# Kernel tuning notes

Measured on AMD Instinct MI355X. Metric: run time of the kernel, lower is better.

## Reference

```python
import jax, jax.numpy as jnp
import numpy as np

N, E, G = 20000, 320000, 1000
F_NODE, F_EDGE, HID, HEADS, NCLS = 12, 4, 64, 4, 4


def setup_inputs() -> dict:
    key = jax.random.key(0)
    ks = iter(jax.random.split(key, 64))

    def rn(shape, s=0.1):
        return jax.random.normal(next(ks), shape, jnp.float32) * s

    inp = {
        "x": rn((N, F_NODE), 1.0),
        "edge_index": jax.random.randint(next(ks), (2, E), 0, N, dtype=jnp.int32),
        "edge_attr": rn((E, F_EDGE), 1.0),
        "batch": jnp.sort(jax.random.randint(next(ks), (N,), 0, G, dtype=jnp.int32)),
    }
    # GATv2 layer params: lin_l (W,b), lin_r (W,b), lin_edge (W, no bias), att, out bias
    for i, (cin, H) in enumerate([(F_NODE, HEADS), (HID * HEADS, HEADS), (HID * HEADS, 1)], 1):
        d = H * HID
        inp[f"Wl{i}"] = rn((cin, d))
        inp[f"bl{i}"] = rn((d,))
        inp[f"Wr{i}"] = rn((cin, d))
        inp[f"br{i}"] = rn((d,))
        inp[f"We{i}"] = rn((F_EDGE, d))
        inp[f"att{i}"] = rn((H, HID))
        inp[f"bias{i}"] = rn((d,))
    inp["mW1"] = rn((HID, 32)); inp["mb1"] = rn((32,))
    inp["mW2"] = rn((32, 16)); inp["mb2"] = rn((16,))
    inp["mW3"] = rn((16, NCLS)); inp["mb3"] = rn((NCLS,))
    return inp


def gatv2(x, src, dst, ea, Wl, bl, Wr, br, We, att, bias, H):
    # PyG GATv2Conv (share_weights=False, negative_slope=0.2, concat=True, eval mode)
    xl = (x @ Wl + bl).reshape(N, H, HID)   # source transform
    xr = (x @ Wr + br).reshape(N, H, HID)   # target transform
    ee = (ea @ We).reshape(E, H, HID)       # edge embedding
    z = jax.nn.leaky_relu(xl[src] + xr[dst] + ee, 0.2)  # [E,H,C]
    logits = jnp.einsum("ehc,hc->eh", z, att)
    m = jax.ops.segment_max(logits, dst, num_segments=N)  # per-dest max
    ex = jnp.exp(logits - m[dst])
    denom = jax.ops.segment_sum(ex, dst, num_segments=N)
    alpha = ex / (denom[dst] + 1e-16)                      # segment softmax
    msg = (xl[src] * alpha[:, :, None]).reshape(E, H * HID)
    out = jax.ops.segment_sum(msg, dst, num_segments=N)
    return out + bias


def reference(x, edge_index, edge_attr, batch,
              Wl1, bl1, Wr1, br1, We1, att1, bias1,
              Wl2, bl2, Wr2, br2, We2, att2, bias2,
              Wl3, bl3, Wr3, br3, We3, att3, bias3,
              mW1, mb1, mW2, mb2, mW3, mb3):
    src, dst = edge_index[0], edge_index[1]
    h = jax.nn.elu(gatv2(x, src, dst, edge_attr, Wl1, bl1, Wr1, br1, We1, att1, bias1, HEADS))
    h = jax.nn.elu(gatv2(h, src, dst, edge_attr, Wl2, bl2, Wr2, br2, We2, att2, bias2, HEADS))
    h = gatv2(h, src, dst, edge_attr, Wl3, bl3, Wr3, br3, We3, att3, bias3, 1)  # [N,HID]
    # global mean pool
    sums = jax.ops.segment_sum(h, batch, num_segments=G)
    cnt = jax.ops.segment_sum(jnp.ones((N, 1), h.dtype), batch, num_segments=G)
    g = sums / jnp.maximum(cnt, 1.0)
    # MLP head (dropout disabled, eval mode)
    g = jax.nn.relu(g @ mW1 + mb1)
    g = jax.nn.relu(g @ mW2 + mb2)
    return g @ mW3 + mb3
```

## Files before the change

kernel.cpp:

```cpp
#include <hip/hip_runtime.h>
#include <hip/hip_bf16.h>

#define NNODES 20000
#define NEDGES 320000
#define NGRAPH 1000

typedef __hip_bfloat16 bf16;
typedef unsigned short u16;
typedef short short8 __attribute__((ext_vector_type(8)));
typedef float f32x4 __attribute__((ext_vector_type(4)));

__device__ __forceinline__ float b2f(bf16 x) { return __bfloat162float(x); }
__device__ __forceinline__ float bu2f(u16 u) { return __uint_as_float(((unsigned)u) << 16); }
__device__ __forceinline__ u16 f2bu(float v) {
    __hip_bfloat16 b = __float2bfloat16(v);
    return *reinterpret_cast<u16*>(&b);
}

__device__ __forceinline__ int idx_at(const void* p, int i, int is64) {
    return is64 ? (int)((const long long*)p)[i] : ((const int*)p)[i];
}

__device__ __forceinline__ float raw_at(const void* p, size_t i, bool isbf) {
    return isbf ? b2f(((const bf16*)p)[i]) : ((const float*)p)[i];
}

static inline char* align16(char* p) {
    return (char*)(((uintptr_t)p + 15) & ~(uintptr_t)15);
}

__global__ void sniff_all(const void* __restrict__ x, const void* __restrict__ ei,
                          const void* __restrict__ batch, int* __restrict__ flags) {
    __shared__ int sb[4];
    if (threadIdx.x < 4) sb[threadIdx.x] = 0;
    __syncthreads();
    int gb = 0, gf = 0, ze = 0, zb = 0;
    for (int i = threadIdx.x; i < 8192; i += blockDim.x) {
        float vb = b2f(((const bf16*)x)[i]);
        float vf = ((const float*)x)[i];
        if (fabsf(vb) < 1e4f) gb++;
        if (fabsf(vf) < 1e4f) gf++;
        if (((const int*)ei)[2 * i + 1] == 0) ze++;
        if (((const int*)batch)[2 * i + 1] == 0) zb++;
    }
    atomicAdd(&sb[0], gb); atomicAdd(&sb[1], gf);
    atomicAdd(&sb[2], ze); atomicAdd(&sb[3], zb);
    __syncthreads();
    if (threadIdx.x == 0) {
        flags[0] = (sb[0] >= sb[1]) ? 1 : 0;
        flags[1] = (sb[2] > 6000) ? 1 : 0;
        flags[2] = (sb[3] > 6000) ? 1 : 0;
    }
}

struct Segs {
    const void* src[29];
    int off[30];
};

__device__ __forceinline__ void wtp_store(u16* __restrict__ dst, const void* __restrict__ src,
                                          int K, int N, int i, bool isbf) {
    int j = i & 7;
    int lane = (i >> 3) & 63;
    int rest = i >> 9;
    int KB = K >> 5;
    int tile = rest / KB, kbi = rest - tile * KB;
    int l16 = lane & 15, quad = lane >> 4;
    int n = tile * 16 + l16;
    int kk = kbi * 32 + quad * 8 + j;
    dst[i] = f2bu(raw_at(src, (size_t)kk * N + n, isbf));
}

__global__ void preprocess(Segs S, const int* __restrict__ flags,
                           float* __restrict__ conv, int total,
                           u16* __restrict__ eah,
                           u16* __restrict__ wt2l, u16* __restrict__ wt2r,
                           u16* __restrict__ wt3l, u16* __restrict__ wt3r,
                           int* __restrict__ deg, float* __restrict__ poolcnt) {
    int i = blockIdx.x * blockDim.x + threadIdx.x;
    bool isbf = flags[0] != 0;
    if (i < total) {
        int lo = 0, hi = 29;
        while (hi - lo > 1) {
            int mid = (lo + hi) >> 1;
            if (i >= S.off[mid]) lo = mid; else hi = mid;
        }
        conv[i] = raw_at(S.src[lo], i - S.off[lo], isbf);
        return;
    }
    i -= total;
    if (i < NEDGES * 4) {
        eah[i] = isbf ? ((const u16*)S.src[1])[i] : f2bu(((const float*)S.src[1])[i]);
        return;
    }
    i -= NEDGES * 4;
    if (i < 65536) { wtp_store(wt2l, S.src[9],  256, 256, i, isbf); return; }
    i -= 65536;
    if (i < 65536) { wtp_store(wt2r, S.src[11], 256, 256, i, isbf); return; }
    i -= 65536;
    if (i < 16384) { wtp_store(wt3l, S.src[16], 256, 64, i, isbf); return; }
    i -= 16384;
    if (i < 16384) { wtp_store(wt3r, S.src[18], 256, 64, i, isbf); return; }
    i -= 16384;
    if (i < NNODES) { deg[i] = 0; return; }
    i -= NNODES;
    if (i < NGRAPH * 65) poolcnt[i] = 0.f;
}

__global__ void csr_hist(const void* __restrict__ ei, const int* __restrict__ flags,
                         int* __restrict__ deg) {
    int e = blockIdx.x * blockDim.x + threadIdx.x;
    if (e >= NEDGES) return;
    atomicAdd(&deg[idx_at(ei, NEDGES + e, flags[1])], 1);
}

__global__ void csr_scan(const int* __restrict__ deg, int* __restrict__ rowptr,
                         int* __restrict__ cursor) {
    __shared__ int wsum[16];
    __shared__ int wpre[16];
    const int t = threadIdx.x;
    const int wid = t >> 6, lane = t & 63;
    const int base = t * 20;
    int loc[20];
    int s = 0;
#pragma unroll
    for (int j = 0; j < 20; j++) {
        int i = base + j;
        int v = (i < NNODES) ? deg[i] : 0;
        loc[j] = s;
        s += v;
    }
    int incl = s;
#pragma unroll
    for (int o = 1; o < 64; o <<= 1) {
        int n = __shfl_up(incl, o);
        if (lane >= o) incl += n;
    }
    if (lane == 63) wsum[wid] = incl;
    __syncthreads();
    if (wid == 0 && lane < 16) {
        int v = wsum[lane];
        int inc2 = v;
#pragma unroll
        for (int o = 1; o < 16; o <<= 1) {
            int n = __shfl_up(inc2, o);
            if (lane >= o) inc2 += n;
        }
        wpre[lane] = inc2 - v;
    }
    __syncthreads();
    int excl = wpre[wid] + incl - s;
#pragma unroll
    for (int j = 0; j < 20; j++) {
        int i = base + j;
        if (i < NNODES) { rowptr[i] = excl + loc[j]; cursor[i] = excl + loc[j]; }
    }
    if (t == 1023) rowptr[NNODES] = excl + s;
}

__global__ void csr_scatter(const void* __restrict__ ei, const int* __restrict__ flags,
                            int* __restrict__ cursor, int2* __restrict__ csr) {
    int e = blockIdx.x * blockDim.x + threadIdx.x;
    if (e >= NEDGES) return;
    const int i64 = flags[1];
    int src = idx_at(ei, e, i64), dst = idx_at(ei, NEDGES + e, i64);
    int pos = atomicAdd(&cursor[dst], 1);
    csr[pos] = make_int2(src, e);
}

template <int TM, int CIN, int DOUT, bool GUARD>
__global__ __launch_bounds__(256, 2) void lin_gemm(
        const float* __restrict__ X,
        const float* __restrict__ Wl, const float* __restrict__ bl,
        const float* __restrict__ Wr, const float* __restrict__ br,
        u16* __restrict__ XL, float* __restrict__ XR) {
    constexpr int CPT = DOUT / 4;
    constexpr int RG = 256 / CPT;
    constexpr int M = RG * TM;
    __shared__ float xs[M * CIN];

    const int t = threadIdx.x;
    const int ct = t % CPT;
    const int rg = t / CPT;
    const int c0 = ct * 4;
    const int r0 = blockIdx.x * M;

    constexpr int C4 = CIN / 4;
    for (int i = t; i < M * C4; i += 256) {
        int r = i / C4, j = i - r * C4;
        float4 v = make_float4(0.f, 0.f, 0.f, 0.f);
        if (!GUARD || (r0 + r) < NNODES)
            v = *(const float4*)&X[(size_t)(r0 + r) * CIN + j * 4];
        *(float4*)&xs[r * CIN + j * 4] = v;
    }
    __syncthreads();

    float4 accL[TM], accR[TM];
#pragma unroll
    for (int m = 0; m < TM; m++) {
        accL[m] = make_float4(0.f, 0.f, 0.f, 0.f);
        accR[m] = make_float4(0.f, 0.f, 0.f, 0.f);
    }
    const float* xbase = &xs[rg * TM * CIN];
#pragma unroll 4
    for (int k = 0; k < CIN; k++) {
        const float4 wl = *(const float4*)&Wl[k * DOUT + c0];
        const float4 wr = *(const float4*)&Wr[k * DOUT + c0];
#pragma unroll
        for (int m = 0; m < TM; m++) {
            float xv = xbase[m * CIN + k];
            accL[m].x = fmaf(xv, wl.x, accL[m].x);
            accL[m].y = fmaf(xv, wl.y, accL[m].y);
            accL[m].z = fmaf(xv, wl.z, accL[m].z);
            accL[m].w = fmaf(xv, wl.w, accL[m].w);
            accR[m].x = fmaf(xv, wr.x, accR[m].x);
            accR[m].y = fmaf(xv, wr.y, accR[m].y);
            accR[m].z = fmaf(xv, wr.z, accR[m].z);
            accR[m].w = fmaf(xv, wr.w, accR[m].w);
        }
    }

    const float4 b4l = *(const float4*)&bl[c0];
    const float4 b4r = *(const float4*)&br[c0];
#pragma unroll
    for (int m = 0; m < TM; m++) {
        int row = r0 + rg * TM + m;
        if (GUARD && row >= NNODES) continue;
        float l0 = accL[m].x + b4l.x, l1 = accL[m].y + b4l.y;
        float l2 = accL[m].z + b4l.z, l3 = accL[m].w + b4l.w;
        uint2 pk;
        pk.x = (unsigned)f2bu(l0) | ((unsigned)f2bu(l1) << 16);
        pk.y = (unsigned)f2bu(l2) | ((unsigned)f2bu(l3) << 16);
        *(uint2*)&XL[(size_t)row * DOUT + c0] = pk;
        float4 r4;
        r4.x = accR[m].x + b4r.x; r4.y = accR[m].y + b4r.y;
        r4.z = accR[m].z + b4r.z; r4.w = accR[m].w + b4r.w;
        *(float4*)&XR[(size_t)row * DOUT + c0] = r4;
    }
}

template <int N>
__global__ __launch_bounds__(256) void lin_gemm_mfma(
        const float* __restrict__ X,
        const u16* __restrict__ WlP, const float* __restrict__ bl,
        const u16* __restrict__ WrP, const float* __restrict__ br,
        u16* __restrict__ XL, float* __restrict__ XR) {
    constexpr int K = 256;
    constexpr int KB = K / 32;
    constexpr int NTW = N / 64;
    constexpr int XSTR = 264;
    __shared__ u16 xhi[16 * XSTR];
    __shared__ u16 xlo[16 * XSTR];

    const int t = threadIdx.x;
    const int w = t >> 6, lane = t & 63;
    const int quad = lane >> 4, l16 = lane & 15;
    const int m0 = blockIdx.x * 16;
    const int nbase = w * (N / 4);

    for (int idx = t; idx < 16 * 64; idx += 256) {
        int r = idx >> 6, c4 = idx & 63;
        float4 v = *(const float4*)&X[(size_t)(m0 + r) * K + c4 * 4];
        float f[4] = {v.x, v.y, v.z, v.w};
        ushort4 hi, lo;
        u16 h;
        h = f2bu(f[0]); hi.x = h; lo.x = f2bu(f[0] - bu2f(h));
        h = f2bu(f[1]); hi.y = h; lo.y = f2bu(f[1] - bu2f(h));
        h = f2bu(f[2]); hi.z = h; lo.z = f2bu(f[2] - bu2f(h));
        h = f2bu(f[3]); hi.w = h; lo.w = f2bu(f[3] - bu2f(h));
        *(ushort4*)&xhi[r * XSTR + c4 * 4] = hi;
        *(ushort4*)&xlo[r * XSTR + c4 * 4] = lo;
    }
    __syncthreads();

    f32x4 accL[NTW], accR[NTW];
#pragma unroll
    for (int i = 0; i < NTW; i++) {
        accL[i] = (f32x4){0.f, 0.f, 0.f, 0.f};
        accR[i] = (f32x4){0.f, 0.f, 0.f, 0.f};
    }

    const int abase = l16 * XSTR + quad * 8;
#pragma unroll
    for (int kbi = 0; kbi < KB; kbi++) {
        short8 ahi = *(const short8*)&xhi[abase + kbi * 32];
        short8 alo = *(const short8*)&xlo[abase + kbi * 32];
#pragma unroll
        for (int i = 0; i < NTW; i++) {
            int tg = (nbase >> 4) + i;
            size_t off = ((size_t)(tg * KB + kbi) * 64 + lane) * 8;
            short8 bL = *(const short8*)&WlP[off];
            short8 bR = *(const short8*)&WrP[off];
            accL[i] = __builtin_amdgcn_mfma_f32_16x16x32_bf16(ahi, bL, accL[i], 0, 0, 0);
            accL[i] = __builtin_amdgcn_mfma_f32_16x16x32_bf16(alo, bL, accL[i], 0, 0, 0);
            accR[i] = __builtin_amdgcn_mfma_f32_16x16x32_bf16(ahi, bR, accR[i], 0, 0, 0);
            accR[i] = __builtin_amdgcn_mfma_f32_16x16x32_bf16(alo, bR, accR[i], 0, 0, 0);
        }
    }

#pragma unroll
    for (int i = 0; i < NTW; i++) {
        int col = nbase + i * 16 + l16;
        float bLv = bl[col], bRv = br[col];
#pragma unroll
        for (int r = 0; r < 4; r++) {
            int row = m0 + quad * 4 + r;
            XL[(size_t)row * N + col] = f2bu(accL[i][r] + bLv);
            XR[(size_t)row * N + col] = accR[i][r] + bRv;
        }
    }
}

template <int H, bool ELU, bool POOLF>
__global__ __launch_bounds__(H * 64, 4) void gat_agg(
                        const int* __restrict__ rowptr, const int2* __restrict__ csr,
                        const u16* __restrict__ XL, const float* __restrict__ XR,
                        const u16* __restrict__ eah,
                        const float* __restrict__ We, const float* __restrict__ att,
                        const float* __restrict__ bias, float* __restrict__ out,
                        const void* __restrict__ batch, const int* __restrict__ flags,
                        float* __restrict__ pool, float* __restrict__ cnt) {
    const int Dout = H * 64;
    const int dst = blockIdx.x;
    const int t = threadIdx.x;
    const int h = t >> 6;
    const int lane = t & 63;
    const int g = lane >> 4;
    const int k = lane & 15;
    const int c0 = h * 64 + k * 4;

    const float4 w0 = *(const float4*)&We[0 * Dout + c0];
    const float4 w1 = *(const float4*)&We[1 * Dout + c0];
    const float4 w2 = *(const float4*)&We[2 * Dout + c0];
    const float4 w3 = *(const float4*)&We[3 * Dout + c0];
    const float4 at = *(const float4*)&att[c0];
    const float4 xr = *(const float4*)&XR[dst * Dout + c0];

    const int i0 = rowptr[dst], i1 = rowptr[dst + 1];
    const int niter = (i1 - i0 + 3) >> 2;

    float l = 0.f;
    float4 acc = make_float4(0.f, 0.f, 0.f, 0.f);

#define GAT_EDGE_BODY(E_IDX)                                                     \
    {                                                                            \
        int e_ = (E_IDX);                                                        \
        bool valid_ = e_ < i1;                                                   \
        int2 se_ = csr[valid_ ? e_ : i0];                                        \
        uint2 xu_ = *(const uint2*)&XL[se_.x * Dout + c0];                       \
        uint2 au_ = *(const uint2*)&eah[se_.y * 4];                              \
        float xl0_ = __uint_as_float(xu_.x << 16);                               \
        float xl1_ = __uint_as_float(xu_.x & 0xffff0000u);                       \
        float xl2_ = __uint_as_float(xu_.y << 16);                               \
        float xl3_ = __uint_as_float(xu_.y & 0xffff0000u);                       \
        float A0_ = __uint_as_float(au_.x << 16);                                \
        float A1_ = __uint_as_float(au_.x & 0xffff0000u);                        \
        float A2_ = __uint_as_float(au_.y << 16);                                \
        float A3_ = __uint_as_float(au_.y & 0xffff0000u);                        \
        float z0_ = fmaf(A0_, w0.x, fmaf(A1_, w1.x, fmaf(A2_, w2.x, fmaf(A3_, w3.x, xl0_ + xr.x)))); \
        float z1_ = fmaf(A0_, w0.y, fmaf(A1_, w1.y, fmaf(A2_, w2.y, fmaf(A3_, w3.y, xl1_ + xr.y)))); \
        float z2_ = fmaf(A0_, w0.z, fmaf(A1_, w1.z, fmaf(A2_, w2.z, fmaf(A3_, w3.z, xl2_ + xr.z)))); \
        float z3_ = fmaf(A0_, w0.w, fmaf(A1_, w1.w, fmaf(A2_, w2.w, fmaf(A3_, w3.w, xl3_ + xr.w)))); \
        z0_ = fmaxf(z0_, 0.2f * z0_);                                            \
        z1_ = fmaxf(z1_, 0.2f * z1_);                                            \
        z2_ = fmaxf(z2_, 0.2f * z2_);                                            \
        z3_ = fmaxf(z3_, 0.2f * z3_);                                            \
        float v_ = fmaf(z3_, at.w, fmaf(z2_, at.z, fmaf(z1_, at.y, z0_ * at.x))); \
        v_ += __shfl_xor(v_, 1);                                                 \
        v_ += __shfl_xor(v_, 2);                                                 \
        v_ += __shfl_xor(v_, 4);                                                 \
        v_ += __shfl_xor(v_, 8);                                                 \
        float p_ = valid_ ? __expf(v_) : 0.f;                                    \
        l += p_;                                                                 \
        acc.x = fmaf(p_, xl0_, acc.x);                                           \
        acc.y = fmaf(p_, xl1_, acc.y);                                           \
        acc.z = fmaf(p_, xl2_, acc.z);                                           \
        acc.w = fmaf(p_, xl3_, acc.w);                                           \
    }

    int it = 0;
    for (; it + 2 <= niter; it += 2) {
        int eb = i0 + g + it * 4;
        GAT_EDGE_BODY(eb)
        GAT_EDGE_BODY(eb + 4)
    }
    if (it < niter) {
        GAT_EDGE_BODY(i0 + g + it * 4)
    }
#undef GAT_EDGE_BODY

    l += __shfl_xor(l, 16);      l += __shfl_xor(l, 32);
    acc.x += __shfl_xor(acc.x, 16); acc.x += __shfl_xor(acc.x, 32);
    acc.y += __shfl_xor(acc.y, 16); acc.y += __shfl_xor(acc.y, 32);
    acc.z += __shfl_xor(acc.z, 16); acc.z += __shfl_xor(acc.z, 32);
    acc.w += __shfl_xor(acc.w, 16); acc.w += __shfl_xor(acc.w, 32);

    if (g == 0) {
        float inv = 1.f / (l + 1e-16f);
        const float4 b4 = *(const float4*)&bias[c0];
        float o0 = fmaf(acc.x, inv, b4.x);
        float o1 = fmaf(acc.y, inv, b4.y);
        float o2 = fmaf(acc.z, inv, b4.z);
        float o3 = fmaf(acc.w, inv, b4.w);
        if (ELU) {
            o0 = o0 > 0.f ? o0 : expf(o0) - 1.f;
            o1 = o1 > 0.f ? o1 : expf(o1) - 1.f;
            o2 = o2 > 0.f ? o2 : expf(o2) - 1.f;
            o3 = o3 > 0.f ? o3 : expf(o3) - 1.f;
        }
        if (POOLF) {
            int b = idx_at(batch, dst, flags[2]);
            atomicAdd(&pool[b * 64 + c0 + 0], o0);
            atomicAdd(&pool[b * 64 + c0 + 1], o1);
            atomicAdd(&pool[b * 64 + c0 + 2], o2);
            atomicAdd(&pool[b * 64 + c0 + 3], o3);
            if (lane == 0) atomicAdd(&cnt[b], 1.f);
        } else {
            *(float4*)&out[dst * Dout + c0] = make_float4(o0, o1, o2, o3);
        }
    }
}

__global__ void mlp_head(const float* __restrict__ pool, const float* __restrict__ cnt,
                         const float* __restrict__ mW1, const float* __restrict__ mb1,
                         const float* __restrict__ mW2, const float* __restrict__ mb2,
                         const float* __restrict__ mW3, const float* __restrict__ mb3,
                         float* __restrict__ out) {
    __shared__ float g[64], s1[32], s2[16];
    int b = blockIdx.x, t = threadIdx.x;
    float c = fmaxf(cnt[b], 1.f);
    g[t] = pool[b * 64 + t] / c;
    __syncthreads();
    if (t < 32) {
        float a = 0.f;
        for (int k = 0; k < 64; k++) a = fmaf(g[k], mW1[k * 32 + t], a);
        s1[t] = fmaxf(a + mb1[t], 0.f);
    }
    __syncthreads();
    if (t < 16) {
        float a = 0.f;
        for (int k = 0; k < 32; k++) a = fmaf(s1[k], mW2[k * 16 + t], a);
        s2[t] = fmaxf(a + mb2[t], 0.f);
    }
    __syncthreads();
    if (t < 4) {
        float a = 0.f;
        for (int k = 0; k < 16; k++) a = fmaf(s2[k], mW3[k * 4 + t], a);
        out[b * 4 + t] = a + mb3[t];
    }
}


extern "C" void kernel_launch(void* const* d_in, const int* in_sizes, int n_in,
                              void* d_out, int out_size, void* d_ws, size_t ws_size,
                              hipStream_t stream) {
    const void* ei    = d_in[1];
    const void* batch = d_in[3];

    int fidx[29];
    fidx[0] = 0;
    fidx[1] = 2;
    for (int i = 0; i < 21; i++) fidx[2 + i] = 4 + i;
    for (int i = 0; i < 6; i++) fidx[23 + i] = 25 + i;

    Segs S;
    int off = 0;
    for (int i = 0; i < 29; i++) {
        S.src[i] = d_in[fidx[i]];
        S.off[i] = off;
        off += in_sizes[fidx[i]];
    }
    S.off[29] = off;
    const int total = off;

    char* p = (char*)d_ws;
    int*   FLAGS  = (int*)p;                 p += 16;
    float* CONV   = (float*)p;               p += sizeof(float) * total;  p = align16(p);
    int*   DEG    = (int*)p;                 p += sizeof(int) * NNODES;
    int*   ROWPTR = (int*)p;                 p += sizeof(int) * (NNODES + 1);
    int*   CURSOR = (int*)p;                 p += sizeof(int) * (NNODES + 1);  p = align16(p);
    int2*  CSR    = (int2*)p;                p += sizeof(int2) * NEDGES;  p = align16(p);
    u16*   EAH    = (u16*)p;                 p += sizeof(u16) * NEDGES * 4;  p = align16(p);
    u16*   WT2L   = (u16*)p;                 p += sizeof(u16) * 256 * 256;
    u16*   WT2R   = (u16*)p;                 p += sizeof(u16) * 256 * 256;
    u16*   WT3L   = (u16*)p;                 p += sizeof(u16) * 64 * 256;
    u16*   WT3R   = (u16*)p;                 p += sizeof(u16) * 64 * 256;  p = align16(p);
    u16*   XLb    = (u16*)p;                 p += sizeof(u16) * NNODES * 256;  p = align16(p);
    float* XRb    = (float*)p;               p += sizeof(float) * NNODES * 256;
    float* ACC    = (float*)p;               p += sizeof(float) * NNODES * 256;
    float* POOL   = (float*)p;               p += sizeof(float) * NGRAPH * 64;
    float* CNT    = (float*)p;               p += sizeof(float) * NGRAPH;

    const float* CX  = CONV + S.off[0];
    const float* CP[21];
    for (int i = 0; i < 21; i++) CP[i] = CONV + S.off[2 + i];
    const float* CmW1 = CONV + S.off[23];
    const float* Cmb1 = CONV + S.off[24];
    const float* CmW2 = CONV + S.off[25];
    const float* Cmb2 = CONV + S.off[26];
    const float* CmW3 = CONV + S.off[27];
    const float* Cmb3 = CONV + S.off[28];

    sniff_all<<<1, 256, 0, stream>>>(d_in[0], ei, batch, FLAGS);
    int pre_total = total + NEDGES * 4 + 65536 * 2 + 16384 * 2 + NNODES + NGRAPH * 65;
    preprocess<<<(pre_total + 255) / 256, 256, 0, stream>>>(
        S, FLAGS, CONV, total, EAH, WT2L, WT2R, WT3L, WT3R, DEG, POOL);

    csr_hist<<<(NEDGES + 255) / 256, 256, 0, stream>>>(ei, FLAGS, DEG);
    csr_scan<<<1, 1024, 0, stream>>>(DEG, ROWPTR, CURSOR);
    csr_scatter<<<(NEDGES + 255) / 256, 256, 0, stream>>>(ei, FLAGS, CURSOR, CSR);

    lin_gemm<4, 12, 256, false><<<NNODES / 16, 256, 0, stream>>>(CX, CP[0], CP[1], CP[2], CP[3], XLb, XRb);
    gat_agg<4, true, false><<<NNODES, 256, 0, stream>>>(ROWPTR, CSR, XLb, XRb, EAH,
        CP[4], CP[5], CP[6], ACC, batch, FLAGS, POOL, CNT);

    lin_gemm_mfma<256><<<NNODES / 16, 256, 0, stream>>>(ACC, WT2L, CP[8], WT2R, CP[10], XLb, XRb);
    gat_agg<4, true, false><<<NNODES, 256, 0, stream>>>(ROWPTR, CSR, XLb, XRb, EAH,
        CP[11], CP[12], CP[13], ACC, batch, FLAGS, POOL, CNT);

    lin_gemm_mfma<64><<<NNODES / 16, 256, 0, stream>>>(ACC, WT3L, CP[15], WT3R, CP[17], XLb, XRb);
    gat_agg<1, false, true><<<NNODES, 64, 0, stream>>>(ROWPTR, CSR, XLb, XRb, EAH,
        CP[18], CP[19], CP[20], ACC, batch, FLAGS, POOL, CNT);

    mlp_head<<<NGRAPH, 64, 0, stream>>>(POOL, CNT, CmW1, Cmb1, CmW2, Cmb2, CmW3, Cmb3, (float*)d_out);
}
```

Baseline: 410.5 us.

## Use wavefront-per-node single-pass GATv2 aggregation for the 4-head layers

```diff
diff --git a/kernel.cpp b/kernel.cpp
--- a/kernel.cpp
+++ b/kernel.cpp
@@ -309,6 +309,86 @@
             XR[(size_t)row * N + col] = accR[i][r] + bRv;
         }
     }
+}
+
+template <bool ELU>
+__global__ __launch_bounds__(256, 4) void gat_agg_mw(
+        const int* __restrict__ rowptr, const int2* __restrict__ csr,
+        const u16* __restrict__ XL, const float* __restrict__ XR,
+        const u16* __restrict__ eah,
+        const float* __restrict__ We, const float* __restrict__ att,
+        const float* __restrict__ bias, float* __restrict__ out) {
+    const int w = threadIdx.x >> 6;
+    const int lane = threadIdx.x & 63;
+    const int dst = blockIdx.x * 4 + w;
+    const int c0 = lane * 4;
+
+    const float4 w0 = *(const float4*)&We[0 * 256 + c0];
+    const float4 w1 = *(const float4*)&We[1 * 256 + c0];
+    const float4 w2 = *(const float4*)&We[2 * 256 + c0];
+    const float4 w3 = *(const float4*)&We[3 * 256 + c0];
+    const float4 at = *(const float4*)&att[c0];
+    const float4 xr = *(const float4*)&XR[(size_t)dst * 256 + c0];
+
+    const int i0 = rowptr[dst], i1 = rowptr[dst + 1];
+
+    float l = 0.f;
+    float4 acc = make_float4(0.f, 0.f, 0.f, 0.f);
+
+    int2 sc = (i0 < i1) ? csr[i0] : make_int2(0, 0);
+    int2 sn = (i0 + 1 < i1) ? csr[i0 + 1] : sc;
+    uint2 xu = *(const uint2*)&XL[(size_t)sc.x * 256 + c0];
+    uint2 au = *(const uint2*)&eah[(size_t)sc.y * 4];
+
+    for (int e = i0; e < i1; ++e) {
+        int2 s2 = (e + 2 < i1) ? csr[e + 2] : sn;
+        uint2 xu_n = *(const uint2*)&XL[(size_t)sn.x * 256 + c0];
+        uint2 au_n = *(const uint2*)&eah[(size_t)sn.y * 4];
+
+        float xl0 = __uint_as_float(xu.x << 16);
+        float xl1 = __uint_as_float(xu.x & 0xffff0000u);
+        float xl2 = __uint_as_float(xu.y << 16);
+        float xl3 = __uint_as_float(xu.y & 0xffff0000u);
+        float A0 = __uint_as_float(au.x << 16);
+        float A1 = __uint_as_float(au.x & 0xffff0000u);
+        float A2 = __uint_as_float(au.y << 16);
+        float A3 = __uint_as_float(au.y & 0xffff0000u);
+        float z0 = fmaf(A0, w0.x, fmaf(A1, w1.x, fmaf(A2, w2.x, fmaf(A3, w3.x, xl0 + xr.x))));
+        float z1 = fmaf(A0, w0.y, fmaf(A1, w1.y, fmaf(A2, w2.y, fmaf(A3, w3.y, xl1 + xr.y))));
+        float z2 = fmaf(A0, w0.z, fmaf(A1, w1.z, fmaf(A2, w2.z, fmaf(A3, w3.z, xl2 + xr.z))));
+        float z3 = fmaf(A0, w0.w, fmaf(A1, w1.w, fmaf(A2, w2.w, fmaf(A3, w3.w, xl3 + xr.w))));
+        z0 = fmaxf(z0, 0.2f * z0);
+        z1 = fmaxf(z1, 0.2f * z1);
+        z2 = fmaxf(z2, 0.2f * z2);
+        z3 = fmaxf(z3, 0.2f * z3);
+        float v = fmaf(z3, at.w, fmaf(z2, at.z, fmaf(z1, at.y, z0 * at.x)));
+        v += __shfl_xor(v, 1);
+        v += __shfl_xor(v, 2);
+        v += __shfl_xor(v, 4);
+        v += __shfl_xor(v, 8);
+        float p = __expf(v);
+        l += p;
+        acc.x = fmaf(p, xl0, acc.x);
+        acc.y = fmaf(p, xl1, acc.y);
+        acc.z = fmaf(p, xl2, acc.z);
+        acc.w = fmaf(p, xl3, acc.w);
+
+        sn = s2; xu = xu_n; au = au_n;
+    }
+
+    float inv = 1.f / (l + 1e-16f);
+    const float4 b4 = *(const float4*)&bias[c0];
+    float o0 = fmaf(acc.x, inv, b4.x);
+    float o1 = fmaf(acc.y, inv, b4.y);
+    float o2 = fmaf(acc.z, inv, b4.z);
+    float o3 = fmaf(acc.w, inv, b4.w);
+    if (ELU) {
+        o0 = o0 > 0.f ? o0 : expf(o0) - 1.f;
+        o1 = o1 > 0.f ? o1 : expf(o1) - 1.f;
+        o2 = o2 > 0.f ? o2 : expf(o2) - 1.f;
+        o3 = o3 > 0.f ? o3 : expf(o3) - 1.f;
+    }
+    *(float4*)&out[(size_t)dst * 256 + c0] = make_float4(o0, o1, o2, o3);
 }
 
 template <int H, bool ELU, bool POOLF>
@@ -511,12 +591,12 @@
     csr_scatter<<<(NEDGES + 255) / 256, 256, 0, stream>>>(ei, FLAGS, CURSOR, CSR);
 
     lin_gemm<4, 12, 256, false><<<NNODES / 16, 256, 0, stream>>>(CX, CP[0], CP[1], CP[2], CP[3], XLb, XRb);
-    gat_agg<4, true, false><<<NNODES, 256, 0, stream>>>(ROWPTR, CSR, XLb, XRb, EAH,
-        CP[4], CP[5], CP[6], ACC, batch, FLAGS, POOL, CNT);
+    gat_agg_mw<true><<<NNODES / 4, 256, 0, stream>>>(ROWPTR, CSR, XLb, XRb, EAH,
+        CP[4], CP[5], CP[6], ACC);
 
     lin_gemm_mfma<256><<<NNODES / 16, 256, 0, stream>>>(ACC, WT2L, CP[8], WT2R, CP[10], XLb, XRb);
-    gat_agg<4, true, false><<<NNODES, 256, 0, stream>>>(ROWPTR, CSR, XLb, XRb, EAH,
-        CP[11], CP[12], CP[13], ACC, batch, FLAGS, POOL, CNT);
+    gat_agg_mw<true><<<NNODES / 4, 256, 0, stream>>>(ROWPTR, CSR, XLb, XRb, EAH,
+        CP[11], CP[12], CP[13], ACC);
 
     lin_gemm_mfma<64><<<NNODES / 16, 256, 0, stream>>>(ACC, WT3L, CP[15], WT3R, CP[17], XLb, XRb);
     gat_agg<1, false, true><<<NNODES, 64, 0, stream>>>(ROWPTR, CSR, XLb, XRb, EAH,
```

After: 434.2 us. 1.06x slower.
